# Kernel tuning notes

Hardware: AMD Instinct MI355X
Metric: run time of the kernel (lower is better)

## Reference

```python
import jax, jax.numpy as jnp
import numpy as np

EMBED = 1024
HEADS = 16
HEAD = EMBED // HEADS
B, S = 8, 1024


def setup_inputs() -> dict:
    key = jax.random.key(0)
    ks = jax.random.split(key, 12)
    inp = {
        "values": jax.random.normal(ks[0], (B, S, EMBED), jnp.float32),
        "keys": jax.random.normal(ks[1], (B, S, EMBED), jnp.float32),
        "query": jax.random.normal(ks[2], (B, S, EMBED), jnp.float32),
        # causal mask broadcastable to [B, heads, q, k]
        "mask": jnp.broadcast_to(jnp.tril(jnp.ones((S, S), jnp.int32))[None, None], (B, 1, S, S)),
        "Wv": jax.random.normal(ks[3], (HEAD, HEAD), jnp.float32) / np.sqrt(HEAD),
        "bv": jnp.zeros((HEAD,), jnp.float32),
        "Wk": jax.random.normal(ks[4], (HEAD, HEAD), jnp.float32) / np.sqrt(HEAD),
        "bk": jnp.zeros((HEAD,), jnp.float32),
        "Wq": jax.random.normal(ks[5], (HEAD, HEAD), jnp.float32) / np.sqrt(HEAD),
        "bq": jnp.zeros((HEAD,), jnp.float32),
        "Wfc": jax.random.normal(ks[6], (EMBED, EMBED), jnp.float32) / np.sqrt(EMBED),
        "bfc": jnp.zeros((EMBED,), jnp.float32),
    }
    return inp


def reference(values, keys, query, mask, Wv, bv, Wk, bk, Wq, bq, Wfc, bfc):
    N, q_len = query.shape[0], query.shape[1]
    k_len, v_len = keys.shape[1], values.shape[1]
    # split heads: [N, S, H, D]
    v = values.reshape(N, v_len, HEADS, HEAD)
    k = keys.reshape(N, k_len, HEADS, HEAD)
    q = query.reshape(N, q_len, HEADS, HEAD)
    # per-head linear projections (torch Linear: x @ W.T + b)
    v = v @ Wv.T + bv
    k = k @ Wk.T + bk
    q = q @ Wq.T + bq
    # scores [N, H, q, k]
    scores = jnp.einsum('nqhz,nkhz->nhqk', q, k)
    scores = jnp.where(mask == 0, -jnp.inf, scores)
    # NOTE: original divides by sqrt(query_size) (sequence length), not head dim
    attn = jax.nn.softmax(scores / jnp.sqrt(jnp.float32(q_len)), axis=-1)
    out = jnp.einsum('nhqk,nkhz->nqhz', attn, v).reshape(N, q_len, HEADS * HEAD)
    return out @ Wfc.T + bfc
```

## Files before the change

### kernel.cpp

```cpp
#include <hip/hip_runtime.h>
#include <stdint.h>

typedef __attribute__((ext_vector_type(8))) short short8;
typedef __attribute__((ext_vector_type(4))) short short4v;
typedef __attribute__((ext_vector_type(4))) float floatx4;
typedef __attribute__((ext_vector_type(4))) unsigned short ushort4v;

#define HEADS 16
#define HEAD 64
#define SEQ 1024
#define BATCH 8

__device__ __forceinline__ unsigned short f2bf(float f) {
    union { float f; unsigned int u; } v; v.f = f;
    unsigned int r = v.u + 0x7FFFu + ((v.u >> 16) & 1u);
    return (unsigned short)(r >> 16);
}

__device__ __forceinline__ void gload_lds16(const void* g, void* l) {
    __builtin_amdgcn_global_load_lds((const __attribute__((address_space(1))) void*)g,
                                     (__attribute__((address_space(3))) void*)l, 16, 0, 0);
}

__global__ __launch_bounds__(256) void cvt_kernel(const float* __restrict__ in,
                                                  unsigned short* __restrict__ out) {
    int i = (blockIdx.x * 256 + threadIdx.x) * 4;
    float4 f = *(const float4*)(in + i);
    ushort4v v;
    v.x = f2bf(f.x); v.y = f2bf(f.y); v.z = f2bf(f.z); v.w = f2bf(f.w);
    *(ushort4v*)(out + i) = v;
}

__global__ __launch_bounds__(256) void proj_kernel(
    const float* __restrict__ Vin, const float* __restrict__ Kin, const float* __restrict__ Qin,
    const float* __restrict__ Wv, const float* __restrict__ bv,
    const float* __restrict__ Wk, const float* __restrict__ bk,
    const float* __restrict__ Wq, const float* __restrict__ bq,
    unsigned short* __restrict__ q_ws, unsigned short* __restrict__ k_ws,
    unsigned short* __restrict__ v_ws)
{
    const int tid = threadIdx.x;
    const int wave = tid >> 6, lane = tid & 63;
    const int lq = lane & 15, quad = lane >> 4;
    const int proj = blockIdx.y;

    const float* X; const float* W; const float* bias;
    if (proj == 0)      { X = Qin; W = Wq; bias = bq; }
    else if (proj == 1) { X = Kin; W = Wk; bias = bk; }
    else                { X = Vin; W = Wv; bias = bv; }

    const int gr0 = blockIdx.x * 16;
    const int h0 = wave * 4;
    const int b = gr0 >> 10, s0 = gr0 & 1023;

    short8 wf[4][2];
#pragma unroll
    for (int nt = 0; nt < 4; ++nt) {
        const float* wr = W + (nt * 16 + lq) * 64 + quad * 8;
#pragma unroll
        for (int ks = 0; ks < 2; ++ks) {
            float4 f0 = *(const float4*)(wr + ks * 32);
            float4 f1 = *(const float4*)(wr + ks * 32 + 4);
            short8 v;
            v[0] = (short)f2bf(f0.x); v[1] = (short)f2bf(f0.y);
            v[2] = (short)f2bf(f0.z); v[3] = (short)f2bf(f0.w);
            v[4] = (short)f2bf(f1.x); v[5] = (short)f2bf(f1.y);
            v[6] = (short)f2bf(f1.z); v[7] = (short)f2bf(f1.w);
            wf[nt][ks] = v;
        }
    }

    const float* xb = X + (size_t)(gr0 + lq) * 1024 + quad * 8;
    const floatx4 zero4 = {0.f, 0.f, 0.f, 0.f};
    const float qscale = 0.03125f * 1.44269504088896340736f;

    if (proj == 2) {
        float bvr[4][4];
#pragma unroll
        for (int nt = 0; nt < 4; ++nt)
#pragma unroll
            for (int r = 0; r < 4; ++r) bvr[nt][r] = bias[nt * 16 + quad * 4 + r];

        unsigned short* vbp = v_ws + (size_t)(b * 16 + h0) * 64 * 1024 + s0 + lq;

        float4 xf[4];
        { const float* p = xb + h0 * 64;
          xf[0] = *(const float4*)p;        xf[1] = *(const float4*)(p + 4);
          xf[2] = *(const float4*)(p + 32); xf[3] = *(const float4*)(p + 36); }
#pragma unroll
        for (int hh = 0; hh < 4; ++hh) {
            float4 xn[4];
            if (hh < 3) {
                const float* p = xb + (h0 + hh + 1) * 64;
                xn[0] = *(const float4*)p;        xn[1] = *(const float4*)(p + 4);
                xn[2] = *(const float4*)(p + 32); xn[3] = *(const float4*)(p + 36);
            }
            short8 aq[2];
#pragma unroll
            for (int ks = 0; ks < 2; ++ks) {
                short8 a;
                a[0] = (short)f2bf(xf[ks * 2].x);     a[1] = (short)f2bf(xf[ks * 2].y);
                a[2] = (short)f2bf(xf[ks * 2].z);     a[3] = (short)f2bf(xf[ks * 2].w);
                a[4] = (short)f2bf(xf[ks * 2 + 1].x); a[5] = (short)f2bf(xf[ks * 2 + 1].y);
                a[6] = (short)f2bf(xf[ks * 2 + 1].z); a[7] = (short)f2bf(xf[ks * 2 + 1].w);
                aq[ks] = a;
            }
            floatx4 acc[4] = {zero4, zero4, zero4, zero4};
#pragma unroll
            for (int ks = 0; ks < 2; ++ks)
#pragma unroll
                for (int nt = 0; nt < 4; ++nt)
                    acc[nt] = __builtin_amdgcn_mfma_f32_16x16x32_bf16(wf[nt][ks], aq[ks], acc[nt], 0, 0, 0);

            unsigned short* vh = vbp + (size_t)hh * 64 * 1024;
#pragma unroll
            for (int nt = 0; nt < 4; ++nt)
#pragma unroll
                for (int r = 0; r < 4; ++r)
                    vh[(size_t)(nt * 16 + quad * 4 + r) * 1024] = f2bf(acc[nt][r] + bvr[nt][r]);
#pragma unroll
            for (int i = 0; i < 4; ++i) xf[i] = xn[i];
        }
    } else {
        float bqk[4];
#pragma unroll
        for (int nt = 0; nt < 4; ++nt) bqk[nt] = bias[nt * 16 + lq];
        const float oscale = (proj == 0) ? qscale : 1.0f;
        unsigned short* dstb = (proj == 0 ? q_ws : k_ws);
        unsigned short* qkp = dstb + ((size_t)((b * 16 + h0) * 1024) + s0 + quad * 4) * 64 + lq;

        float4 xf[4];
        { const float* p = xb + h0 * 64;
          xf[0] = *(const float4*)p;        xf[1] = *(const float4*)(p + 4);
          xf[2] = *(const float4*)(p + 32); xf[3] = *(const float4*)(p + 36); }
#pragma unroll
        for (int hh = 0; hh < 4; ++hh) {
            float4 xn[4];
            if (hh < 3) {
                const float* p = xb + (h0 + hh + 1) * 64;
                xn[0] = *(const float4*)p;        xn[1] = *(const float4*)(p + 4);
                xn[2] = *(const float4*)(p + 32); xn[3] = *(const float4*)(p + 36);
            }
            short8 aq[2];
#pragma unroll
            for (int ks = 0; ks < 2; ++ks) {
                short8 a;
                a[0] = (short)f2bf(xf[ks * 2].x);     a[1] = (short)f2bf(xf[ks * 2].y);
                a[2] = (short)f2bf(xf[ks * 2].z);     a[3] = (short)f2bf(xf[ks * 2].w);
                a[4] = (short)f2bf(xf[ks * 2 + 1].x); a[5] = (short)f2bf(xf[ks * 2 + 1].y);
                a[6] = (short)f2bf(xf[ks * 2 + 1].z); a[7] = (short)f2bf(xf[ks * 2 + 1].w);
                aq[ks] = a;
            }
            floatx4 acc[4] = {zero4, zero4, zero4, zero4};
#pragma unroll
            for (int ks = 0; ks < 2; ++ks)
#pragma unroll
                for (int nt = 0; nt < 4; ++nt)
                    acc[nt] = __builtin_amdgcn_mfma_f32_16x16x32_bf16(aq[ks], wf[nt][ks], acc[nt], 0, 0, 0);

            unsigned short* qh = qkp + (size_t)hh * 1024 * 64;
#pragma unroll
            for (int nt = 0; nt < 4; ++nt)
#pragma unroll
                for (int r = 0; r < 4; ++r) {
                    float ov = (acc[nt][r] + bqk[nt]) * oscale;
                    qh[r * 64 + nt * 16] = f2bf(ov);
                }
#pragma unroll
            for (int i = 0; i < 4; ++i) xf[i] = xn[i];
        }
    }
}

__global__ __launch_bounds__(256, 2) void attn_kernel(
    const unsigned short* __restrict__ q_ws, const unsigned short* __restrict__ k_ws,
    const unsigned short* __restrict__ v_ws, unsigned short* __restrict__ attn_ws)
{
    const int bh = blockIdx.x;
    const int b = bh >> 4, h = bh & 15;
    const int tid = threadIdx.x;
    const int wave = tid >> 6, lane = tid & 63;
    const int lq = lane & 15, quad = lane >> 4;
    const int r8 = lane >> 3, ch = lane & 7;
    const int sw = ch ^ r8;

    __shared__ unsigned short sK[64 * 64];
    __shared__ unsigned short sV[64 * 64];
    __shared__ unsigned short sP[4][32 * 64];

    const size_t head_off = (size_t)bh * SEQ * HEAD;
    const unsigned short* qb = q_ws + head_off;
    const unsigned short* kb = k_ws + head_off;
    const unsigned short* vb = v_ws + head_off;

    short8 ones;
#pragma unroll
    for (int j = 0; j < 8; ++j) ones[j] = (short)0x3F80;

    const floatx4 zero4 = {0.f, 0.f, 0.f, 0.f};

    for (int pass = 0; pass < 2; ++pass) {
        const int qt = pass ? (7 - blockIdx.y) : blockIdx.y;
        const int q0 = qt * 128;
        const int q_lo = q0 + wave * 32;
        const int q_hi = q_lo + 31;
        const int nkt = 2 * qt + 2;

        short8 aq[2][2];
#pragma unroll
        for (int rg = 0; rg < 2; ++rg) {
            const unsigned short* qp = qb + (size_t)(q0 + wave * 32 + rg * 16 + lq) * 64 + quad * 8;
            aq[rg][0] = *(const short8*)qp;
            aq[rg][1] = *(const short8*)(qp + 32);
        }

        floatx4 o[2][4];
        floatx4 lacc[2] = {zero4, zero4};
#pragma unroll
        for (int rg = 0; rg < 2; ++rg)
#pragma unroll
            for (int nt = 0; nt < 4; ++nt) o[rg][nt] = zero4;

        for (int kt = 0; kt < nkt; ++kt) {
#pragma unroll
            for (int i = 0; i < 2; ++i) {
                int br = wave * 16 + i * 8;
                const char* gK = (const char*)(kb + (size_t)(kt * 64 + br + r8) * 64) + sw * 16;
                gload_lds16(gK, (char*)sK + br * 128);
                const char* gV = (const char*)(vb + (size_t)(br + r8) * 1024 + kt * 64) + sw * 16;
                gload_lds16(gV, (char*)sV + br * 128);
            }
            __syncthreads();

            const bool skip = (kt * 64 > q_hi);
            if (!skip) {
                const bool full = (kt * 64 + 63 <= q_lo);

                floatx4 s[2][4];
#pragma unroll
                for (int rg = 0; rg < 2; ++rg)
#pragma unroll
                    for (int nt = 0; nt < 4; ++nt) s[rg][nt] = zero4;
#pragma unroll
                for (int ks = 0; ks < 2; ++ks) {
#pragma unroll
                    for (int nt = 0; nt < 4; ++nt) {
                        short8 kf = *(const short8*)(sK + (nt * 16 + lq) * 64 +
                                                     (((quad + 4 * ks) ^ (lq & 7)) * 8));
                        s[0][nt] = __builtin_amdgcn_mfma_f32_16x16x32_bf16(aq[0][ks], kf, s[0][nt], 0, 0, 0);
                        s[1][nt] = __builtin_amdgcn_mfma_f32_16x16x32_bf16(aq[1][ks], kf, s[1][nt], 0, 0, 0);
                    }
                }

                unsigned short* wp = &sP[wave][0];
#pragma unroll
                for (int rg = 0; rg < 2; ++rg) {
#pragma unroll
                    for (int nt = 0; nt < 4; ++nt) {
                        int kcol = kt * 64 + nt * 16 + lq;
                        int chn = (((nt * 2 + (lq >> 3)) ^ (quad << 1)) * 8) + (lq & 7);
#pragma unroll
                        for (int r = 0; r < 4; ++r) {
                            float p = __builtin_amdgcn_exp2f(s[rg][nt][r]);
                            if (!full) {
                                int qrow = q_lo + rg * 16 + quad * 4 + r;
                                if (kcol > qrow) p = 0.f;
                            }
                            wp[(rg * 16 + quad * 4 + r) * 64 + chn] = f2bf(p);
                        }
                    }
                }

                short8 vf[4][2];
#pragma unroll
                for (int nt = 0; nt < 4; ++nt)
#pragma unroll
                    for (int ks = 0; ks < 2; ++ks)
                        vf[nt][ks] = *(const short8*)(sV + (nt * 16 + lq) * 64 +
                                                      (((quad + 4 * ks) ^ (lq & 7)) * 8));
#pragma unroll
                for (int rg = 0; rg < 2; ++rg) {
#pragma unroll
                    for (int ks = 0; ks < 2; ++ks) {
                        short8 pa = *(const short8*)&sP[wave][(rg * 16 + lq) * 64 +
                                     (((ks * 4 + quad) ^ (((lq >> 2) & 3) << 1)) * 8)];
                        lacc[rg] = __builtin_amdgcn_mfma_f32_16x16x32_bf16(pa, ones, lacc[rg], 0, 0, 0);
#pragma unroll
                        for (int nt = 0; nt < 4; ++nt)
                            o[rg][nt] = __builtin_amdgcn_mfma_f32_16x16x32_bf16(pa, vf[nt][ks], o[rg][nt], 0, 0, 0);
                    }
                }
            }
            __syncthreads();
        }

#pragma unroll
        for (int rg = 0; rg < 2; ++rg) {
            float inv[4];
#pragma unroll
            for (int r = 0; r < 4; ++r) inv[r] = 1.f / lacc[rg][r];
            const int srow_base = q0 + wave * 32 + rg * 16 + quad * 4;
#pragma unroll
            for (int nt = 0; nt < 4; ++nt) {
                int col = h * 64 + nt * 16 + lq;
#pragma unroll
                for (int r = 0; r < 4; ++r) {
                    attn_ws[((size_t)(b * SEQ + srow_base + r)) * 1024 + col] = f2bf(o[rg][nt][r] * inv[r]);
                }
            }
        }
    }
}

__global__ __launch_bounds__(256) void fc_kernel(
    const unsigned short* __restrict__ A, const unsigned short* __restrict__ Bw,
    const float* __restrict__ bias, float* __restrict__ out)
{
    const int nt0 = blockIdx.x * 128;
    const int mt0 = blockIdx.y * 128;
    const int tid = threadIdx.x;
    const int wave = tid >> 6, lane = tid & 63;
    const int lq = lane & 15, quad = lane >> 4;
    const int wm = (wave >> 1) * 64, wn = (wave & 1) * 64;

    __shared__ unsigned short sA[128 * 32];
    __shared__ unsigned short sB[128 * 32];

    const floatx4 zero4 = {0.f, 0.f, 0.f, 0.f};
    floatx4 acc[4][4];
#pragma unroll
    for (int i = 0; i < 4; ++i)
#pragma unroll
        for (int j = 0; j < 4; ++j) acc[i][j] = zero4;

    for (int kt = 0; kt < 32; ++kt) {
#pragma unroll
        for (int issue = 0; issue < 2; ++issue) {
            int off = (issue * 4 + wave) * 1024 + lane * 16;
            int row = off >> 6;
            int cb = off & 63;
            const char* ga = (const char*)A + (size_t)(mt0 + row) * 2048 + kt * 64 + cb;
            gload_lds16(ga, (char*)sA + (issue * 4 + wave) * 1024);
            const char* gb = (const char*)Bw + (size_t)(nt0 + row) * 2048 + kt * 64 + cb;
            gload_lds16(gb, (char*)sB + (issue * 4 + wave) * 1024);
        }
        __syncthreads();

        short8 af[4], bf[4];
#pragma unroll
        for (int i = 0; i < 4; ++i) {
            af[i] = *(const short8*)(sA + (wm + i * 16 + lq) * 32 + quad * 8);
            bf[i] = *(const short8*)(sB + (wn + i * 16 + lq) * 32 + quad * 8);
        }
#pragma unroll
        for (int mi = 0; mi < 4; ++mi)
#pragma unroll
            for (int ni = 0; ni < 4; ++ni)
                acc[mi][ni] = __builtin_amdgcn_mfma_f32_16x16x32_bf16(af[mi], bf[ni], acc[mi][ni], 0, 0, 0);
        __syncthreads();
    }

#pragma unroll
    for (int mi = 0; mi < 4; ++mi) {
#pragma unroll
        for (int ni = 0; ni < 4; ++ni) {
            int col = nt0 + wn + ni * 16 + lq;
            float bc = bias[col];
#pragma unroll
            for (int r = 0; r < 4; ++r) {
                int row = mt0 + wm + mi * 16 + quad * 4 + r;
                out[(size_t)row * 1024 + col] = acc[mi][ni][r] + bc;
            }
        }
    }
}

extern "C" void kernel_launch(void* const* d_in, const int* in_sizes, int n_in,
                              void* d_out, int out_size, void* d_ws, size_t ws_size,
                              hipStream_t stream)
{
    const float* values = (const float*)d_in[0];
    const float* keys   = (const float*)d_in[1];
    const float* query  = (const float*)d_in[2];
    const float* Wv  = (const float*)d_in[4];
    const float* bv  = (const float*)d_in[5];
    const float* Wk  = (const float*)d_in[6];
    const float* bk  = (const float*)d_in[7];
    const float* Wq  = (const float*)d_in[8];
    const float* bq  = (const float*)d_in[9];
    const float* Wfc = (const float*)d_in[10];
    const float* bfc = (const float*)d_in[11];
    float* out = (float*)d_out;

    char* ws = (char*)d_ws;
    unsigned short* q_ws    = (unsigned short*)(ws);
    unsigned short* k_ws    = (unsigned short*)(ws + (16u << 20));
    unsigned short* v_ws    = (unsigned short*)(ws + (32u << 20));
    unsigned short* attn_ws = (unsigned short*)(ws + (48u << 20));
    unsigned short* wfc_ws  = (unsigned short*)(ws + (64u << 20));

    cvt_kernel<<<dim3(1024), dim3(256), 0, stream>>>(Wfc, wfc_ws);
    proj_kernel<<<dim3(512, 3), dim3(256), 0, stream>>>(
        values, keys, query, Wv, bv, Wk, bk, Wq, bq, q_ws, k_ws, v_ws);
    attn_kernel<<<dim3(128, 4), dim3(256), 0, stream>>>(q_ws, k_ws, v_ws, attn_ws);
    fc_kernel<<<dim3(8, 64), dim3(256), 0, stream>>>(attn_ws, wfc_ws, bfc, out);
}
```

Measured before the change: 261.2 us.

## Stage projection outputs through LDS, split attention passes, deepen FC k-tile

The projection kernel now writes its Q/K/V tiles into a per-wave shared-memory buffer, then stores them to global memory as contiguous 16-byte vectors instead of scattered 2-byte stores. The attention kernel drops its two-pass balanced loop in favour of one q-tile per block. The grid doubles and the launch bound rises to 4 blocks, trading load balance for more parallelism. The FC GEMM doubles its K tile to 64 with an XOR-swizzled LDS layout, halving the barrier count at the cost of more shared memory.

New measurement: 262.9 us. Within noise of the previous version (+0.6%).

```diff
diff --git a/kernel.cpp b/kernel.cpp
--- a/kernel.cpp
+++ b/kernel.cpp
@@ -53,6 +53,8 @@
     const int h0 = wave * 4;
     const int b = gr0 >> 10, s0 = gr0 & 1023;
 
+    __shared__ unsigned short sT[4][1280];
+
     short8 wf[4][2];
 #pragma unroll
     for (int nt = 0; nt < 4; ++nt) {
@@ -72,7 +74,6 @@
 
     const float* xb = X + (size_t)(gr0 + lq) * 1024 + quad * 8;
     const floatx4 zero4 = {0.f, 0.f, 0.f, 0.f};
-    const float qscale = 0.03125f * 1.44269504088896340736f;
 
     if (proj == 2) {
         float bvr[4][4];
@@ -81,7 +82,10 @@
 #pragma unroll
             for (int r = 0; r < 4; ++r) bvr[nt][r] = bias[nt * 16 + quad * 4 + r];
 
-        unsigned short* vbp = v_ws + (size_t)(b * 16 + h0) * 64 * 1024 + s0 + lq;
+        unsigned short* tw = &sT[wave][0];
+        const int rrow = lane >> 1, rhalf = lane & 1;
+        const unsigned short* tr0 = &sT[wave][rrow * 20 + rhalf * 8];
+        const unsigned short* tr1 = &sT[wave][(rrow + 32) * 20 + rhalf * 8];
 
         float4 xf[4];
         { const float* p = xb + h0 * 64;
@@ -112,12 +116,18 @@
                 for (int nt = 0; nt < 4; ++nt)
                     acc[nt] = __builtin_amdgcn_mfma_f32_16x16x32_bf16(wf[nt][ks], aq[ks], acc[nt], 0, 0, 0);
 
-            unsigned short* vh = vbp + (size_t)hh * 64 * 1024;
 #pragma unroll
             for (int nt = 0; nt < 4; ++nt)
 #pragma unroll
                 for (int r = 0; r < 4; ++r)
-                    vh[(size_t)(nt * 16 + quad * 4 + r) * 1024] = f2bf(acc[nt][r] + bvr[nt][r]);
+                    tw[(nt * 16 + quad * 4 + r) * 20 + lq] = f2bf(acc[nt][r] + bvr[nt][r]);
+
+            short8 o0 = *(const short8*)tr0;
+            short8 o1 = *(const short8*)tr1;
+            unsigned short* vh = v_ws + (size_t)((b * 16 + h0 + hh) * 64) * 1024 + s0 + rhalf * 8;
+            *(short8*)(vh + (size_t)rrow * 1024) = o0;
+            *(short8*)(vh + (size_t)(rrow + 32) * 1024) = o1;
+
 #pragma unroll
             for (int i = 0; i < 4; ++i) xf[i] = xn[i];
         }
@@ -125,9 +135,12 @@
         float bqk[4];
 #pragma unroll
         for (int nt = 0; nt < 4; ++nt) bqk[nt] = bias[nt * 16 + lq];
-        const float oscale = (proj == 0) ? qscale : 1.0f;
-        unsigned short* dstb = (proj == 0 ? q_ws : k_ws);
-        unsigned short* qkp = dstb + ((size_t)((b * 16 + h0) * 1024) + s0 + quad * 4) * 64 + lq;
+        const float qscale = 0.03125f * 1.44269504088896340736f;
+        const float oscale = proj ? 1.0f : qscale;
+        unsigned short* dstb = proj ? k_ws : q_ws;
+
+        unsigned short* tw = &sT[wave][0];
+        const unsigned short* tr = &sT[wave][(lane >> 2) * 68 + (lane & 3) * 16];
 
         float4 xf[4];
         { const float* p = xb + h0 * 64;
@@ -158,21 +171,25 @@
                 for (int nt = 0; nt < 4; ++nt)
                     acc[nt] = __builtin_amdgcn_mfma_f32_16x16x32_bf16(aq[ks], wf[nt][ks], acc[nt], 0, 0, 0);
 
-            unsigned short* qh = qkp + (size_t)hh * 1024 * 64;
 #pragma unroll
             for (int nt = 0; nt < 4; ++nt)
 #pragma unroll
-                for (int r = 0; r < 4; ++r) {
-                    float ov = (acc[nt][r] + bqk[nt]) * oscale;
-                    qh[r * 64 + nt * 16] = f2bf(ov);
-                }
+                for (int r = 0; r < 4; ++r)
+                    tw[(quad * 4 + r) * 68 + nt * 16 + lq] = f2bf((acc[nt][r] + bqk[nt]) * oscale);
+
+            short8 o0 = *(const short8*)tr;
+            short8 o1 = *(const short8*)(tr + 8);
+            unsigned short* dst = dstb + ((size_t)((b * 16 + h0 + hh) * 1024) + s0) * 64 + lane * 16;
+            *(short8*)dst = o0;
+            *(short8*)(dst + 8) = o1;
+
 #pragma unroll
             for (int i = 0; i < 4; ++i) xf[i] = xn[i];
         }
     }
 }
 
-__global__ __launch_bounds__(256, 2) void attn_kernel(
+__global__ __launch_bounds__(256, 4) void attn_kernel(
     const unsigned short* __restrict__ q_ws, const unsigned short* __restrict__ k_ws,
     const unsigned short* __restrict__ v_ws, unsigned short* __restrict__ attn_ws)
 {
@@ -199,114 +216,112 @@
 
     const floatx4 zero4 = {0.f, 0.f, 0.f, 0.f};
 
-    for (int pass = 0; pass < 2; ++pass) {
-        const int qt = pass ? (7 - blockIdx.y) : blockIdx.y;
-        const int q0 = qt * 128;
-        const int q_lo = q0 + wave * 32;
-        const int q_hi = q_lo + 31;
-        const int nkt = 2 * qt + 2;
-
-        short8 aq[2][2];
-#pragma unroll
-        for (int rg = 0; rg < 2; ++rg) {
-            const unsigned short* qp = qb + (size_t)(q0 + wave * 32 + rg * 16 + lq) * 64 + quad * 8;
-            aq[rg][0] = *(const short8*)qp;
-            aq[rg][1] = *(const short8*)(qp + 32);
-        }
-
-        floatx4 o[2][4];
-        floatx4 lacc[2] = {zero4, zero4};
-#pragma unroll
-        for (int rg = 0; rg < 2; ++rg)
-#pragma unroll
-            for (int nt = 0; nt < 4; ++nt) o[rg][nt] = zero4;
-
-        for (int kt = 0; kt < nkt; ++kt) {
-#pragma unroll
-            for (int i = 0; i < 2; ++i) {
-                int br = wave * 16 + i * 8;
-                const char* gK = (const char*)(kb + (size_t)(kt * 64 + br + r8) * 64) + sw * 16;
-                gload_lds16(gK, (char*)sK + br * 128);
-                const char* gV = (const char*)(vb + (size_t)(br + r8) * 1024 + kt * 64) + sw * 16;
-                gload_lds16(gV, (char*)sV + br * 128);
-            }
-            __syncthreads();
-
-            const bool skip = (kt * 64 > q_hi);
-            if (!skip) {
-                const bool full = (kt * 64 + 63 <= q_lo);
-
-                floatx4 s[2][4];
-#pragma unroll
-                for (int rg = 0; rg < 2; ++rg)
-#pragma unroll
-                    for (int nt = 0; nt < 4; ++nt) s[rg][nt] = zero4;
-#pragma unroll
-                for (int ks = 0; ks < 2; ++ks) {
-#pragma unroll
-                    for (int nt = 0; nt < 4; ++nt) {
-                        short8 kf = *(const short8*)(sK + (nt * 16 + lq) * 64 +
-                                                     (((quad + 4 * ks) ^ (lq & 7)) * 8));
-                        s[0][nt] = __builtin_amdgcn_mfma_f32_16x16x32_bf16(aq[0][ks], kf, s[0][nt], 0, 0, 0);
-                        s[1][nt] = __builtin_amdgcn_mfma_f32_16x16x32_bf16(aq[1][ks], kf, s[1][nt], 0, 0, 0);
+    const int qt = blockIdx.y;
+    const int q0 = qt * 128;
+    const int q_lo = q0 + wave * 32;
+    const int q_hi = q_lo + 31;
+    const int nkt = 2 * qt + 2;
+
+    short8 aq[2][2];
+#pragma unroll
+    for (int rg = 0; rg < 2; ++rg) {
+        const unsigned short* qp = qb + (size_t)(q0 + wave * 32 + rg * 16 + lq) * 64 + quad * 8;
+        aq[rg][0] = *(const short8*)qp;
+        aq[rg][1] = *(const short8*)(qp + 32);
+    }
+
+    floatx4 o[2][4];
+    floatx4 lacc[2] = {zero4, zero4};
+#pragma unroll
+    for (int rg = 0; rg < 2; ++rg)
+#pragma unroll
+        for (int nt = 0; nt < 4; ++nt) o[rg][nt] = zero4;
+
+    for (int kt = 0; kt < nkt; ++kt) {
+#pragma unroll
+        for (int i = 0; i < 2; ++i) {
+            int br = wave * 16 + i * 8;
+            const char* gK = (const char*)(kb + (size_t)(kt * 64 + br + r8) * 64) + sw * 16;
+            gload_lds16(gK, (char*)sK + br * 128);
+            const char* gV = (const char*)(vb + (size_t)(br + r8) * 1024 + kt * 64) + sw * 16;
+            gload_lds16(gV, (char*)sV + br * 128);
+        }
+        __syncthreads();
+
+        const bool skip = (kt * 64 > q_hi);
+        if (!skip) {
+            const bool full = (kt * 64 + 63 <= q_lo);
+
+            floatx4 s[2][4];
+#pragma unroll
+            for (int rg = 0; rg < 2; ++rg)
+#pragma unroll
+                for (int nt = 0; nt < 4; ++nt) s[rg][nt] = zero4;
+#pragma unroll
+            for (int ks = 0; ks < 2; ++ks) {
+#pragma unroll
+                for (int nt = 0; nt < 4; ++nt) {
+                    short8 kf = *(const short8*)(sK + (nt * 16 + lq) * 64 +
+                                                 (((quad + 4 * ks) ^ (lq & 7)) * 8));
+                    s[0][nt] = __builtin_amdgcn_mfma_f32_16x16x32_bf16(aq[0][ks], kf, s[0][nt], 0, 0, 0);
+                    s[1][nt] = __builtin_amdgcn_mfma_f32_16x16x32_bf16(aq[1][ks], kf, s[1][nt], 0, 0, 0);
+                }
+            }
+
+            unsigned short* wp = &sP[wave][0];
+#pragma unroll
+            for (int rg = 0; rg < 2; ++rg) {
+#pragma unroll
+                for (int nt = 0; nt < 4; ++nt) {
+                    int kcol = kt * 64 + nt * 16 + lq;
+                    int chn = (((nt * 2 + (lq >> 3)) ^ (quad << 1)) * 8) + (lq & 7);
+#pragma unroll
+                    for (int r = 0; r < 4; ++r) {
+                        float p = __builtin_amdgcn_exp2f(s[rg][nt][r]);
+                        if (!full) {
+                            int qrow = q_lo + rg * 16 + quad * 4 + r;
+                            if (kcol > qrow) p = 0.f;
+                        }
+                        wp[(rg * 16 + quad * 4 + r) * 64 + chn] = f2bf(p);
                     }
                 }
-
-                unsigned short* wp = &sP[wave][0];
-#pragma unroll
-                for (int rg = 0; rg < 2; ++rg) {
-#pragma unroll
-                    for (int nt = 0; nt < 4; ++nt) {
-                        int kcol = kt * 64 + nt * 16 + lq;
-                        int chn = (((nt * 2 + (lq >> 3)) ^ (quad << 1)) * 8) + (lq & 7);
-#pragma unroll
-                        for (int r = 0; r < 4; ++r) {
-                            float p = __builtin_amdgcn_exp2f(s[rg][nt][r]);
-                            if (!full) {
-                                int qrow = q_lo + rg * 16 + quad * 4 + r;
-                                if (kcol > qrow) p = 0.f;
-                            }
-                            wp[(rg * 16 + quad * 4 + r) * 64 + chn] = f2bf(p);
-                        }
-                    }
+            }
+
+            short8 vf[4][2];
+#pragma unroll
+            for (int nt = 0; nt < 4; ++nt)
+#pragma unroll
+                for (int ks = 0; ks < 2; ++ks)
+                    vf[nt][ks] = *(const short8*)(sV + (nt * 16 + lq) * 64 +
+                                                  (((quad + 4 * ks) ^ (lq & 7)) * 8));
+#pragma unroll
+            for (int rg = 0; rg < 2; ++rg) {
+#pragma unroll
+                for (int ks = 0; ks < 2; ++ks) {
+                    short8 pa = *(const short8*)&sP[wave][(rg * 16 + lq) * 64 +
+                                 (((ks * 4 + quad) ^ (((lq >> 2) & 3) << 1)) * 8)];
+                    lacc[rg] = __builtin_amdgcn_mfma_f32_16x16x32_bf16(pa, ones, lacc[rg], 0, 0, 0);
+#pragma unroll
+                    for (int nt = 0; nt < 4; ++nt)
+                        o[rg][nt] = __builtin_amdgcn_mfma_f32_16x16x32_bf16(pa, vf[nt][ks], o[rg][nt], 0, 0, 0);
                 }
-
-                short8 vf[4][2];
-#pragma unroll
-                for (int nt = 0; nt < 4; ++nt)
-#pragma unroll
-                    for (int ks = 0; ks < 2; ++ks)
-                        vf[nt][ks] = *(const short8*)(sV + (nt * 16 + lq) * 64 +
-                                                      (((quad + 4 * ks) ^ (lq & 7)) * 8));
-#pragma unroll
-                for (int rg = 0; rg < 2; ++rg) {
-#pragma unroll
-                    for (int ks = 0; ks < 2; ++ks) {
-                        short8 pa = *(const short8*)&sP[wave][(rg * 16 + lq) * 64 +
-                                     (((ks * 4 + quad) ^ (((lq >> 2) & 3) << 1)) * 8)];
-                        lacc[rg] = __builtin_amdgcn_mfma_f32_16x16x32_bf16(pa, ones, lacc[rg], 0, 0, 0);
-#pragma unroll
-                        for (int nt = 0; nt < 4; ++nt)
-                            o[rg][nt] = __builtin_amdgcn_mfma_f32_16x16x32_bf16(pa, vf[nt][ks], o[rg][nt], 0, 0, 0);
-                    }
-                }
-            }
-            __syncthreads();
-        }
-
-#pragma unroll
-        for (int rg = 0; rg < 2; ++rg) {
-            float inv[4];
-#pragma unroll
-            for (int r = 0; r < 4; ++r) inv[r] = 1.f / lacc[rg][r];
-            const int srow_base = q0 + wave * 32 + rg * 16 + quad * 4;
-#pragma unroll
-            for (int nt = 0; nt < 4; ++nt) {
-                int col = h * 64 + nt * 16 + lq;
-#pragma unroll
-                for (int r = 0; r < 4; ++r) {
-                    attn_ws[((size_t)(b * SEQ + srow_base + r)) * 1024 + col] = f2bf(o[rg][nt][r] * inv[r]);
-                }
+            }
+        }
+        __syncthreads();
+    }
+
+#pragma unroll
+    for (int rg = 0; rg < 2; ++rg) {
+        float inv[4];
+#pragma unroll
+        for (int r = 0; r < 4; ++r) inv[r] = 1.f / lacc[rg][r];
+        const int srow_base = q0 + wave * 32 + rg * 16 + quad * 4;
+#pragma unroll
+        for (int nt = 0; nt < 4; ++nt) {
+            int col = h * 64 + nt * 16 + lq;
+#pragma unroll
+            for (int r = 0; r < 4; ++r) {
+                attn_ws[((size_t)(b * SEQ + srow_base + r)) * 1024 + col] = f2bf(o[rg][nt][r] * inv[r]);
             }
         }
     }
@@ -323,8 +338,8 @@
     const int lq = lane & 15, quad = lane >> 4;
     const int wm = (wave >> 1) * 64, wn = (wave & 1) * 64;
 
-    __shared__ unsigned short sA[128 * 32];
-    __shared__ unsigned short sB[128 * 32];
+    __shared__ unsigned short sA[128 * 64];
+    __shared__ unsigned short sB[128 * 64];
 
     const floatx4 zero4 = {0.f, 0.f, 0.f, 0.f};
     floatx4 acc[4][4];
@@ -333,30 +348,37 @@
 #pragma unroll
         for (int j = 0; j < 4; ++j) acc[i][j] = zero4;
 
-    for (int kt = 0; kt < 32; ++kt) {
-#pragma unroll
-        for (int issue = 0; issue < 2; ++issue) {
-            int off = (issue * 4 + wave) * 1024 + lane * 16;
-            int row = off >> 6;
-            int cb = off & 63;
-            const char* ga = (const char*)A + (size_t)(mt0 + row) * 2048 + kt * 64 + cb;
-            gload_lds16(ga, (char*)sA + (issue * 4 + wave) * 1024);
-            const char* gb = (const char*)Bw + (size_t)(nt0 + row) * 2048 + kt * 64 + cb;
-            gload_lds16(gb, (char*)sB + (issue * 4 + wave) * 1024);
+    const int sc = (tid & 7) ^ ((tid >> 3) & 7);
+    const int sr = tid >> 3;
+
+    for (int kt = 0; kt < 16; ++kt) {
+#pragma unroll
+        for (int j = 0; j < 4; ++j) {
+            int r = j * 32 + sr;
+            const char* ga = (const char*)A + (size_t)(mt0 + r) * 2048 + kt * 128 + sc * 16;
+            gload_lds16(ga, (char*)sA + (j * 256 + tid) * 16);
+            const char* gb = (const char*)Bw + (size_t)(nt0 + r) * 2048 + kt * 128 + sc * 16;
+            gload_lds16(gb, (char*)sB + (j * 256 + tid) * 16);
         }
         __syncthreads();
 
-        short8 af[4], bf[4];
-#pragma unroll
-        for (int i = 0; i < 4; ++i) {
-            af[i] = *(const short8*)(sA + (wm + i * 16 + lq) * 32 + quad * 8);
-            bf[i] = *(const short8*)(sB + (wn + i * 16 + lq) * 32 + quad * 8);
-        }
-#pragma unroll
-        for (int mi = 0; mi < 4; ++mi)
-#pragma unroll
-            for (int ni = 0; ni < 4; ++ni)
-                acc[mi][ni] = __builtin_amdgcn_mfma_f32_16x16x32_bf16(af[mi], bf[ni], acc[mi][ni], 0, 0, 0);
+        short8 af[4][2], bf[4][2];
+#pragma unroll
+        for (int i = 0; i < 4; ++i)
+#pragma unroll
+            for (int ks = 0; ks < 2; ++ks) {
+                af[i][ks] = *(const short8*)(sA + (wm + i * 16 + lq) * 64 +
+                                             (((quad + 4 * ks) ^ (lq & 7)) * 8));
+                bf[i][ks] = *(const short8*)(sB + (wn + i * 16 + lq) * 64 +
+                                             (((quad + 4 * ks) ^ (lq & 7)) * 8));
+            }
+#pragma unroll
+        for (int ks = 0; ks < 2; ++ks)
+#pragma unroll
+            for (int mi = 0; mi < 4; ++mi)
+#pragma unroll
+                for (int ni = 0; ni < 4; ++ni)
+                    acc[mi][ni] = __builtin_amdgcn_mfma_f32_16x16x32_bf16(af[mi][ks], bf[ni][ks], acc[mi][ni], 0, 0, 0);
         __syncthreads();
     }
 
@@ -402,6 +424,6 @@
     cvt_kernel<<<dim3(1024), dim3(256), 0, stream>>>(Wfc, wfc_ws);
     proj_kernel<<<dim3(512, 3), dim3(256), 0, stream>>>(
         values, keys, query, Wv, bv, Wk, bk, Wq, bq, q_ws, k_ws, v_ws);
-    attn_kernel<<<dim3(128, 4), dim3(256), 0, stream>>>(q_ws, k_ws, v_ws, attn_ws);
+    attn_kernel<<<dim3(128, 8), dim3(256), 0, stream>>>(q_ws, k_ws, v_ws, attn_ws);
     fc_kernel<<<dim3(8, 64), dim3(256), 0, stream>>>(attn_ws, wfc_ws, bfc, out);
 }
```
